# Performance work log

Hardware: AMD Instinct MI355X
Metric: run time of the kernel (lower is better)

The kernel has to match this reference:

```python
import jax, jax.numpy as jnp
import numpy as np

FEAT = 9
H = 128
L = 2
NH = 4
EPS = 1e-5


def _ln(v, g, b):
    m = v.mean(-1, keepdims=True)
    var = ((v - m) ** 2).mean(-1, keepdims=True)
    return (v - m) * jax.lax.rsqrt(var + EPS) * g + b


def _grn(x, fc1_w, fc1_b, fc2_w, fc2_b, gate_w, gate_b, ln_g, ln_b, skip_w=None, skip_b=None):
    h1 = jax.nn.elu(x @ fc1_w.T + fc1_b)
    h = h1 @ fc2_w.T + fc2_b
    g = jax.nn.sigmoid(h1 @ gate_w.T + gate_b)
    s = x if skip_w is None else x @ skip_w.T + skip_b
    return _ln(s + h * g, ln_g, ln_b)


def _lstm(xs, wih, whh, bih, bhh, h0, c0):
    # xs: [B,T,I]; PyTorch gate order i,f,g,o
    pre = jnp.einsum('bti,gi->btg', xs, wih) + bih  # hoist input projection out of scan

    def step(carry, p):
        h, c = carry
        gates = p + h @ whh.T + bhh
        i, f, g, o = jnp.split(gates, 4, axis=-1)
        c = jax.nn.sigmoid(f) * c + jax.nn.sigmoid(i) * jnp.tanh(g)
        h = jax.nn.sigmoid(o) * jnp.tanh(c)
        return (h, c), h

    (h, c), ys = jax.lax.scan(step, (h0, c0), jnp.swapaxes(pre, 0, 1))
    return jnp.swapaxes(ys, 0, 1), h, c


def _mha(q, k, v, in_w, in_b, out_w, out_b):
    B, Tq, _ = q.shape
    Tk = k.shape[1]
    dh = H // NH
    wq, wk, wv = jnp.split(in_w, 3, axis=0)
    bq, bk, bv = jnp.split(in_b, 3, axis=0)
    Q = (q @ wq.T + bq).reshape(B, Tq, NH, dh)
    K = (k @ wk.T + bk).reshape(B, Tk, NH, dh)
    V = (v @ wv.T + bv).reshape(B, Tk, NH, dh)
    a = jnp.einsum('bqhd,bkhd->bhqk', Q, K) * (dh ** -0.5)
    a = jax.nn.softmax(a, axis=-1)
    o = jnp.einsum('bhqk,bkhd->bqhd', a, V).reshape(B, Tq, H)
    return o @ out_w.T + out_b


def _forward(x, vsn_fc1_w, vsn_fc1_b, vsn_fc2_w, vsn_fc2_b, vsn_gate_w, vsn_gate_b,
             vsn_skip_w, vsn_skip_b, vsn_ln_g, vsn_ln_b,
             gc_fc1_w, gc_fc1_b, gc_fc2_w, gc_fc2_b, gc_gate_w, gc_gate_b,
             gc_skip_w, gc_skip_b, gc_ln_g, gc_ln_b,
             enc_wih, enc_whh, enc_bih, enc_bhh,
             dec_wih, dec_whh, dec_bih, dec_bhh,
             attn_in_w, attn_in_b, attn_out_w, attn_out_b,
             pa_fc1_w, pa_fc1_b, pa_fc2_w, pa_fc2_b, pa_gate_w, pa_gate_b, pa_ln_g, pa_ln_b,
             fo_w, fo_b, encoder_steps, forecast_steps):
    B = x.shape[0]
    # --- VariableSelectionNetwork, batched over (batch * time) instead of per-timestep loop ---
    xe = x[:, :encoder_steps, :].reshape(B * encoder_steps, FEAT)  # [N,9]
    # per-feature GRNs with input_dim=1: fc1 weight is a column vector -> broadcast multiply
    h1 = jax.nn.elu(xe[:, :, None] * vsn_fc1_w[None] + vsn_fc1_b[None])  # [N,9,128]
    h = jnp.einsum('nfi,foi->nfo', h1, vsn_fc2_w) + vsn_fc2_b
    g = jax.nn.sigmoid(jnp.einsum('nfi,foi->nfo', h1, vsn_gate_w) + vsn_gate_b)
    s = xe[:, :, None] * vsn_skip_w[None] + vsn_skip_b[None]
    proc = _ln(s + h * g, vsn_ln_g, vsn_ln_b)  # [N,9,128]
    sel = _grn(proc.reshape(-1, FEAT * H), gc_fc1_w, gc_fc1_b, gc_fc2_w, gc_fc2_b,
               gc_gate_w, gc_gate_b, gc_ln_g, gc_ln_b, gc_skip_w, gc_skip_b)  # [N,128]
    enc_in = sel.reshape(B, encoder_steps, H)
    # --- 2-layer encoder LSTM ---
    z = jnp.zeros((B, H), x.dtype)
    y = enc_in
    hs, cs = [], []
    for l in range(L):
        y, hh, cc = _lstm(y, enc_wih[l], enc_whh[l], enc_bih[l], enc_bhh[l], z, z)
        hs.append(hh)
        cs.append(cc)
    enc_out = y  # [B,168,128]
    # --- decoder: last encoder output repeated, init state from encoder ---
    dec_in = jnp.repeat(enc_out[:, -1:, :], forecast_steps, axis=1)
    y = dec_in
    for l in range(L):
        y, _, _ = _lstm(y, dec_wih[l], dec_whh[l], dec_bih[l], dec_bhh[l], hs[l], cs[l])
    # --- cross attention decoder -> encoder ---
    attn = _mha(y, enc_out, enc_out, attn_in_w, attn_in_b, attn_out_w, attn_out_b)
    a = _grn(attn.reshape(-1, H), pa_fc1_w, pa_fc1_b, pa_fc2_w, pa_fc2_b,
             pa_gate_w, pa_gate_b, pa_ln_g, pa_ln_b)
    a = a.reshape(B, forecast_steps, H)
    return a @ fo_w.T + fo_b  # [B,24,6] (6 per-output linears fused)


def setup_inputs() -> dict:
    key = jax.random.key(0)
    ks = iter(jax.random.split(key, 64))

    def rn(*s):
        return jax.random.normal(next(ks), s, dtype=jnp.float32) * 0.05

    B = 256
    return dict(
        x=jax.random.normal(next(ks), (B, 168, FEAT), dtype=jnp.float32),
        vsn_fc1_w=rn(FEAT, H), vsn_fc1_b=rn(FEAT, H),
        vsn_fc2_w=rn(FEAT, H, H), vsn_fc2_b=rn(FEAT, H),
        vsn_gate_w=rn(FEAT, H, H), vsn_gate_b=rn(FEAT, H),
        vsn_skip_w=rn(FEAT, H), vsn_skip_b=rn(FEAT, H),
        vsn_ln_g=jnp.ones((FEAT, H), jnp.float32), vsn_ln_b=jnp.zeros((FEAT, H), jnp.float32),
        gc_fc1_w=rn(H, FEAT * H), gc_fc1_b=rn(H),
        gc_fc2_w=rn(H, H), gc_fc2_b=rn(H),
        gc_gate_w=rn(H, H), gc_gate_b=rn(H),
        gc_skip_w=rn(H, FEAT * H), gc_skip_b=rn(H),
        gc_ln_g=jnp.ones((H,), jnp.float32), gc_ln_b=jnp.zeros((H,), jnp.float32),
        enc_wih=rn(L, 4 * H, H), enc_whh=rn(L, 4 * H, H), enc_bih=rn(L, 4 * H), enc_bhh=rn(L, 4 * H),
        dec_wih=rn(L, 4 * H, H), dec_whh=rn(L, 4 * H, H), dec_bih=rn(L, 4 * H), dec_bhh=rn(L, 4 * H),
        attn_in_w=rn(3 * H, H), attn_in_b=rn(3 * H),
        attn_out_w=rn(H, H), attn_out_b=rn(H),
        pa_fc1_w=rn(H, H), pa_fc1_b=rn(H),
        pa_fc2_w=rn(H, H), pa_fc2_b=rn(H),
        pa_gate_w=rn(H, H), pa_gate_b=rn(H),
        pa_ln_g=jnp.ones((H,), jnp.float32), pa_ln_b=jnp.zeros((H,), jnp.float32),
        fo_w=rn(6, H), fo_b=rn(6),
        encoder_steps=168, forecast_steps=24,
    )


def reference(x, vsn_fc1_w, vsn_fc1_b, vsn_fc2_w, vsn_fc2_b, vsn_gate_w, vsn_gate_b,
              vsn_skip_w, vsn_skip_b, vsn_ln_g, vsn_ln_b,
              gc_fc1_w, gc_fc1_b, gc_fc2_w, gc_fc2_b, gc_gate_w, gc_gate_b,
              gc_skip_w, gc_skip_b, gc_ln_g, gc_ln_b,
              enc_wih, enc_whh, enc_bih, enc_bhh,
              dec_wih, dec_whh, dec_bih, dec_bhh,
              attn_in_w, attn_in_b, attn_out_w, attn_out_b,
              pa_fc1_w, pa_fc1_b, pa_fc2_w, pa_fc2_b, pa_gate_w, pa_gate_b, pa_ln_g, pa_ln_b,
              fo_w, fo_b, encoder_steps, forecast_steps):
    return _forward(x, vsn_fc1_w, vsn_fc1_b, vsn_fc2_w, vsn_fc2_b, vsn_gate_w, vsn_gate_b,
                    vsn_skip_w, vsn_skip_b, vsn_ln_g, vsn_ln_b,
                    gc_fc1_w, gc_fc1_b, gc_fc2_w, gc_fc2_b, gc_gate_w, gc_gate_b,
                    gc_skip_w, gc_skip_b, gc_ln_g, gc_ln_b,
                    enc_wih, enc_whh, enc_bih, enc_bhh,
                    dec_wih, dec_whh, dec_bih, dec_bhh,
                    attn_in_w, attn_in_b, attn_out_w, attn_out_b,
                    pa_fc1_w, pa_fc1_b, pa_fc2_w, pa_fc2_b, pa_gate_w, pa_gate_b, pa_ln_g, pa_ln_b,
                    fo_w, fo_b, encoder_steps, forecast_steps)
```

## Files before the change

### kernel.cpp

```cpp
#include <hip/hip_runtime.h>
#include <hip/hip_bf16.h>

#define NBATCH 256
#define TSE 168
#define TSD 24
#define NTOK (NBATCH*TSE)
#define NDTOK (NBATCH*TSD)

#define OFF_PA_FC1T    0
#define OFF_PA_FC2T    16384
#define OFF_PA_GATET   32768

#define PK_VSN   0
#define PK_GC1   294912
#define PK_GC2   589824
#define PK_ENC0  622592
#define PK_ENC1  688128
#define PK_DEC0  753664
#define PK_DEC1  819200
#define PK_AIN   884736
#define PK_AOUT  933888

typedef __attribute__((ext_vector_type(8))) short short8;
typedef __attribute__((ext_vector_type(4))) float f32x4;
typedef __attribute__((ext_vector_type(2))) __fp16 fp16x2;

__device__ __forceinline__ float sigm(float x){ return 1.f/(1.f + __expf(-x)); }
__device__ __forceinline__ float tanhx(float x){
  float cx = fminf(fmaxf(x, -15.f), 15.f);
  float e = __expf(2.f*cx);
  return (e-1.f)/(e+1.f);
}
__device__ __forceinline__ float eluf(float x){ return x > 0.f ? x : (__expf(x)-1.f); }
__device__ __forceinline__ unsigned short f2bu(float v){
  unsigned int u = __float_as_uint(v);
  u = (u + 0x7fffu + ((u>>16)&1u)) >> 16;
  return (unsigned short)u;
}
__device__ __forceinline__ unsigned int pkh(float a, float b){
  union { fp16x2 h; unsigned int u; } v;
  v.h = __builtin_amdgcn_cvt_pkrtz(a, b);
  return v.u;
}
__device__ __forceinline__ unsigned short f2h(float x){
  union { _Float16 h; unsigned short u; } v;
  v.h = (_Float16)x; return v.u;
}
__device__ __forceinline__ float h2f(unsigned short u){
  union { unsigned short u; _Float16 h; } v;
  v.u = u; return (float)v.h;
}
__device__ __forceinline__ float fd2(unsigned int a, unsigned int b, float c){
  union { unsigned int u; fp16x2 h; } ua, ub;
  ua.u = a; ub.u = b;
  return __builtin_amdgcn_fdot2(ua.h, ub.h, c, false);
}

__global__ __launch_bounds__(256) void k_transpose3(float* __restrict__ wtp,
    const float* s0, const float* s1, const float* s2)
{
  int idx = blockIdx.x*256 + threadIdx.x;
  if (idx >= 49152) return;
  int s = idx >> 14, li = idx & 16383;
  int r = li >> 7, c = li & 127;
  const float* src = (s == 0) ? s0 : (s == 1) ? s1 : s2;
  wtp[s*16384 + c*128 + r] = src[li];
}

__global__ __launch_bounds__(256) void k_pack(
    const float* __restrict__ s0, const float* __restrict__ s1,
    unsigned short* __restrict__ dst, int K, int NC, int nsplit,
    int s0bs, int s1bs, int dstbs)
{
  int id = blockIdx.x*256 + threadIdx.x;
  if (id >= K*NC) return;
  int by = blockIdx.y;
  int n = id / K, k = id - n*K;
  float v = (n < nsplit) ? s0[(size_t)by*s0bs + (size_t)n*K + k]
                         : s1[(size_t)by*s1bs + (size_t)(n-nsplit)*K + k];
  int ct = n >> 4, kc = k >> 5;
  int lane = (n & 15) | (((k >> 3) & 3) << 4);
  int j = k & 7;
  int KC = K >> 5;
  dst[(size_t)by*dstbs + (((size_t)ct*KC + kc)*64 + lane)*8 + j] = f2bu(v);
}

__global__ __launch_bounds__(256) void k_vsn_mfma(
    const float* __restrict__ x, const float* __restrict__ fc1_w, const float* __restrict__ fc1_b,
    const unsigned short* __restrict__ pk, const float* __restrict__ fc2_b,
    const float* __restrict__ gate_b, const float* __restrict__ skip_w,
    const float* __restrict__ skip_b, const float* __restrict__ ln_g,
    const float* __restrict__ ln_b, unsigned short* __restrict__ proc2)
{
  const int f = blockIdx.y;
  const int nb = blockIdx.x;
  const int n0 = nb * 64;
  const int tid = threadIdx.x;
  const int wv = tid >> 6, l = tid & 63;
  __shared__ __align__(16) unsigned short As[64*136];
  __shared__ float xs[64];
  __shared__ float vbuf[64*129];
  __shared__ float red[64][4][2];
  __shared__ float mr[64][2];
  if (tid < 64) xs[tid] = x[(size_t)(n0+tid)*9 + f];
  __syncthreads();
  { int i = tid & 127;
    float w1 = fc1_w[f*128 + i], b1 = fc1_b[f*128 + i];
    for (int it = 0; it < 32; it++) {
      int tk = (tid >> 7) + it*2;
      As[tk*136 + i] = f2bu(eluf(xs[tk]*w1 + b1));
    }
  }
  __syncthreads();
  const unsigned short* Wp = pk + PK_VSN + (size_t)f*32768;
  f32x4 acc[4][4];
  #pragma unroll
  for (int rt = 0; rt < 4; rt++)
    #pragma unroll
    for (int ci = 0; ci < 4; ci++) acc[rt][ci] = (f32x4)(0.f);
  #pragma unroll
  for (int kc = 0; kc < 4; kc++) {
    short8 af[4];
    #pragma unroll
    for (int rt = 0; rt < 4; rt++) {
      int row = rt*16 + (l & 15), g = kc*4 + (l >> 4);
      af[rt] = *(const short8*)&As[row*136 + g*8];
    }
    short8 bf[4];
    #pragma unroll
    for (int ci = 0; ci < 4; ci++) {
      int ct = (ci < 2) ? (wv*2 + ci) : (8 + wv*2 + (ci-2));
      bf[ci] = *(const short8*)&Wp[(((size_t)ct*4 + kc)*64 + l)*8];
    }
    #pragma unroll
    for (int rt = 0; rt < 4; rt++)
      #pragma unroll
      for (int ci = 0; ci < 4; ci++)
        acc[rt][ci] = __builtin_amdgcn_mfma_f32_16x16x32_bf16(af[rt], bf[ci], acc[rt][ci], 0, 0, 0);
  }
  __syncthreads();
  #pragma unroll
  for (int ci = 0; ci < 2; ci++) {
    int ch = wv*32 + ci*16 + (l & 15);
    float fb = fc2_b[f*128 + ch], gb = gate_b[f*128 + ch];
    float sw = skip_w[f*128 + ch], sb = skip_b[f*128 + ch];
    #pragma unroll
    for (int rt = 0; rt < 4; rt++)
      #pragma unroll
      for (int r = 0; r < 4; r++) {
        int row = rt*16 + (l >> 4)*4 + r;
        float hv = acc[rt][ci][r] + fb;
        float gv = sigm(acc[rt][ci+2][r] + gb);
        float sv = xs[row]*sw + sb;
        vbuf[row*129 + ch] = sv + hv*gv;
      }
  }
  __syncthreads();
  { int tk = tid >> 2, q = tid & 3;
    float s1 = 0.f, s2 = 0.f;
    #pragma unroll
    for (int i = 0; i < 32; i++) { float z = vbuf[tk*129 + q*32 + i]; s1 += z; s2 += z*z; }
    red[tk][q][0] = s1; red[tk][q][1] = s2;
  }
  __syncthreads();
  if ((tid & 3) == 0) {
    int tk = tid >> 2;
    float a = 0.f, b2 = 0.f;
    for (int p = 0; p < 4; p++) { a += red[tk][p][0]; b2 += red[tk][p][1]; }
    float mean = a * 0.0078125f;
    float var = b2 * 0.0078125f - mean*mean;
    mr[tk][0] = mean; mr[tk][1] = rsqrtf(fmaxf(var, 0.f) + 1e-5f);
  }
  __syncthreads();
  { int i = tid & 127;
    float lg = ln_g[f*128 + i], lb = ln_b[f*128 + i];
    size_t base = ((size_t)nb*9 + f)*8192;
    for (int it = 0; it < 32; it++) {
      int tk = (tid >> 7) + it*2;
      float z = (vbuf[tk*129 + i] - mr[tk][0]) * mr[tk][1] * lg + lb;
      proc2[base + tk*128 + i] = f2bu(z);
    }
  }
}

__global__ __launch_bounds__(256) void k_gc_mfma(
    const unsigned short* __restrict__ proc2, const unsigned short* __restrict__ pk,
    const float* __restrict__ fc1_b, const float* __restrict__ fc2_b,
    const float* __restrict__ gate_b, const float* __restrict__ skip_b,
    const float* __restrict__ ln_g, const float* __restrict__ ln_b,
    unsigned short* __restrict__ selb)
{
  const int nb = blockIdx.x;
  const int n0 = nb * 64;
  const int tid = threadIdx.x;
  const int wv = tid >> 6, l = tid & 63;
  __shared__ __align__(16) unsigned short As[64*136];
  __shared__ __align__(16) unsigned short A2s[64*136];
  __shared__ float vbuf[64*129];
  __shared__ float red[64][4][2];
  __shared__ float mr[64][2];
  const unsigned short* W1 = pk + PK_GC1;
  f32x4 acc1[4][4];
  #pragma unroll
  for (int rt = 0; rt < 4; rt++)
    #pragma unroll
    for (int ci = 0; ci < 4; ci++) acc1[rt][ci] = (f32x4)(0.f);
  for (int c = 0; c < 9; c++) {
    size_t cbase = ((size_t)nb*9 + c)*8192;
    #pragma unroll
    for (int i = 0; i < 4; i++) {
      int gi = i*256 + tid;
      int row = gi >> 4, g = gi & 15;
      uint4 v = *(const uint4*)(proc2 + cbase + row*128 + g*8);
      *(uint4*)&As[row*136 + g*8] = v;
    }
    __syncthreads();
    #pragma unroll
    for (int kc = 0; kc < 4; kc++) {
      int kk = c*4 + kc;
      short8 af[4];
      #pragma unroll
      for (int rt = 0; rt < 4; rt++) {
        int row = rt*16 + (l & 15), g = kc*4 + (l >> 4);
        af[rt] = *(const short8*)&As[row*136 + g*8];
      }
      short8 bf[4];
      #pragma unroll
      for (int ci = 0; ci < 4; ci++) {
        int ct = (ci < 2) ? (wv*2 + ci) : (8 + wv*2 + (ci-2));
        bf[ci] = *(const short8*)&W1[(((size_t)ct*36 + kk)*64 + l)*8];
      }
      #pragma unroll
      for (int rt = 0; rt < 4; rt++)
        #pragma unroll
        for (int ci = 0; ci < 4; ci++)
          acc1[rt][ci] = __builtin_amdgcn_mfma_f32_16x16x32_bf16(af[rt], bf[ci], acc1[rt][ci], 0, 0, 0);
    }
    __syncthreads();
  }
  #pragma unroll
  for (int ci = 0; ci < 2; ci++) {
    int ch = wv*32 + ci*16 + (l & 15);
    float fb = fc1_b[ch];
    #pragma unroll
    for (int rt = 0; rt < 4; rt++)
      #pragma unroll
      for (int r = 0; r < 4; r++) {
        int row = rt*16 + (l >> 4)*4 + r;
        A2s[row*136 + ch] = f2bu(eluf(acc1[rt][ci][r] + fb));
      }
  }
  __syncthreads();
  const unsigned short* W2 = pk + PK_GC2;
  f32x4 acc2[4][4];
  #pragma unroll
  for (int rt = 0; rt < 4; rt++)
    #pragma unroll
    for (int ci = 0; ci < 4; ci++) acc2[rt][ci] = (f32x4)(0.f);
  #pragma unroll
  for (int kc = 0; kc < 4; kc++) {
    short8 af[4];
    #pragma unroll
    for (int rt = 0; rt < 4; rt++) {
      int row = rt*16 + (l & 15), g = kc*4 + (l >> 4);
      af[rt] = *(const short8*)&A2s[row*136 + g*8];
    }
    short8 bf[4];
    #pragma unroll
    for (int ci = 0; ci < 4; ci++) {
      int ct = (ci < 2) ? (wv*2 + ci) : (8 + wv*2 + (ci-2));
      bf[ci] = *(const short8*)&W2[(((size_t)ct*4 + kc)*64 + l)*8];
    }
    #pragma unroll
    for (int rt = 0; rt < 4; rt++)
      #pragma unroll
      for (int ci = 0; ci < 4; ci++)
        acc2[rt][ci] = __builtin_amdgcn_mfma_f32_16x16x32_bf16(af[rt], bf[ci], acc2[rt][ci], 0, 0, 0);
  }
  __syncthreads();
  #pragma unroll
  for (int ci = 0; ci < 2; ci++) {
    int ch = wv*32 + ci*16 + (l & 15);
    float f2 = fc2_b[ch], gb = gate_b[ch], sb = skip_b[ch];
    #pragma unroll
    for (int rt = 0; rt < 4; rt++)
      #pragma unroll
      for (int r = 0; r < 4; r++) {
        int row = rt*16 + (l >> 4)*4 + r;
        float hv = acc2[rt][ci][r] + f2;
        float gv = sigm(acc2[rt][ci+2][r] + gb);
        float sv = acc1[rt][ci+2][r] + sb;
        vbuf[row*129 + ch] = sv + hv*gv;
      }
  }
  __syncthreads();
  { int tk = tid >> 2, q = tid & 3;
    float s1 = 0.f, s2 = 0.f;
    #pragma unroll
    for (int i = 0; i < 32; i++) { float z = vbuf[tk*129 + q*32 + i]; s1 += z; s2 += z*z; }
    red[tk][q][0] = s1; red[tk][q][1] = s2;
  }
  __syncthreads();
  if ((tid & 3) == 0) {
    int tk = tid >> 2;
    float a = 0.f, b2 = 0.f;
    for (int p = 0; p < 4; p++) { a += red[tk][p][0]; b2 += red[tk][p][1]; }
    float mean = a * 0.0078125f;
    float var = b2 * 0.0078125f - mean*mean;
    mr[tk][0] = mean; mr[tk][1] = rsqrtf(fmaxf(var, 0.f) + 1e-5f);
  }
  __syncthreads();
  { int i = tid & 127;
    float lg = ln_g[i], lb = ln_b[i];
    for (int it = 0; it < 32; it++) {
      int tk = (tid >> 7) + it*2;
      float z = (vbuf[tk*129 + i] - mr[tk][0]) * mr[tk][1] * lg + lb;
      selb[(size_t)(n0+tk)*128 + i] = f2bu(z);
    }
  }
}

__global__ __launch_bounds__(256) void k_mm(
    const unsigned short* __restrict__ A, const unsigned short* __restrict__ Wp,
    const float* __restrict__ b0, const float* __restrict__ b1,
    void* __restrict__ out, int out_ld, int outmode)
{
  const int r0 = blockIdx.x * 64;
  const int cb = blockIdx.y * 128;
  const int tid = threadIdx.x;
  const int wv = tid >> 6, l = tid & 63;
  __shared__ __align__(16) unsigned short As[64*136];
  #pragma unroll
  for (int i = 0; i < 4; i++) {
    int gi = i*256 + tid;
    int row = gi >> 4, g = gi & 15;
    uint4 v = *(const uint4*)(A + (size_t)(r0+row)*128 + g*8);
    *(uint4*)&As[row*136 + g*8] = v;
  }
  __syncthreads();
  f32x4 acc[4][2];
  #pragma unroll
  for (int rt = 0; rt < 4; rt++)
    #pragma unroll
    for (int ci = 0; ci < 2; ci++) acc[rt][ci] = (f32x4)(0.f);
  #pragma unroll
  for (int kc = 0; kc < 4; kc++) {
    short8 af[4];
    #pragma unroll
    for (int rt = 0; rt < 4; rt++) {
      int row = rt*16 + (l & 15), g = kc*4 + (l >> 4);
      af[rt] = *(const short8*)&As[row*136 + g*8];
    }
    short8 bf[2];
    #pragma unroll
    for (int ci = 0; ci < 2; ci++) {
      int ct = (cb >> 4) + wv*2 + ci;
      bf[ci] = *(const short8*)&Wp[(((size_t)ct*4 + kc)*64 + l)*8];
    }
    #pragma unroll
    for (int rt = 0; rt < 4; rt++)
      #pragma unroll
      for (int ci = 0; ci < 2; ci++)
        acc[rt][ci] = __builtin_amdgcn_mfma_f32_16x16x32_bf16(af[rt], bf[ci], acc[rt][ci], 0, 0, 0);
  }
  #pragma unroll
  for (int ci = 0; ci < 2; ci++) {
    int cl = cb + wv*32 + ci*16 + (l & 15);
    float bias = b0[cl] + (b1 ? b1[cl] : 0.f);
    #pragma unroll
    for (int rt = 0; rt < 4; rt++)
      #pragma unroll
      for (int r = 0; r < 4; r++) {
        int row = r0 + rt*16 + (l >> 4)*4 + r;
        float v = acc[rt][ci][r] + bias;
        if (outmode == 0) ((float*)out)[(size_t)row*out_ld + cl] = v;
        else ((unsigned short*)out)[(size_t)row*out_ld + cl] = f2h(v);
      }
  }
}

__global__ __launch_bounds__(256, 1) void k_lscan(
    const unsigned short* __restrict__ pre,
    const float* __restrict__ whh,
    const float* __restrict__ h0i, const float* __restrict__ c0i,
    int T, int tstr,
    unsigned short* __restrict__ ys,
    float* __restrict__ hT, float* __restrict__ cT,
    unsigned short* __restrict__ hTb)
{
  const int b = blockIdx.x, tid = threadIdx.x;
  unsigned int w0[64], w1[64];
  {
    const float* p0 = whh + (size_t)tid*128;
    const float* p1 = whh + (size_t)(tid+256)*128;
    #pragma unroll
    for (int k = 0; k < 64; k++) {
      w0[k] = pkh(p0[2*k], p0[2*k+1]);
      w1[k] = pkh(p1[2*k], p1[2*k+1]);
    }
  }
  __shared__ __align__(16) unsigned short hs[128];
  __shared__ float fg[256];
  float c = 0.f;
  if (tid < 128) {
    float h = h0i ? h0i[(size_t)b*128 + tid] : 0.f;
    c = c0i ? c0i[(size_t)b*128 + tid] : 0.f;
    hs[tid] = f2h(h);
  }
  __syncthreads();
  const unsigned short* preb = pre + (size_t)b * (tstr ? (size_t)T*tstr : 512);
  for (int t = 0; t < T; t++) {
    const unsigned short* pt = preb + (size_t)t*tstr;
    unsigned short p0 = pt[tid], p1 = pt[256 + tid];
    float a0[4] = {0.f,0.f,0.f,0.f}, a1[4] = {0.f,0.f,0.f,0.f};
    #pragma unroll
    for (int k4 = 0; k4 < 16; k4++) {
      uint4 hh = *(const uint4*)&hs[k4*8];
      a0[0] = fd2(w0[4*k4+0], hh.x, a0[0]);
      a0[1] = fd2(w0[4*k4+1], hh.y, a0[1]);
      a0[2] = fd2(w0[4*k4+2], hh.z, a0[2]);
      a0[3] = fd2(w0[4*k4+3], hh.w, a0[3]);
      a1[0] = fd2(w1[4*k4+0], hh.x, a1[0]);
      a1[1] = fd2(w1[4*k4+1], hh.y, a1[1]);
      a1[2] = fd2(w1[4*k4+2], hh.z, a1[2]);
      a1[3] = fd2(w1[4*k4+3], hh.w, a1[3]);
    }
    float g0 = h2f(p0) + (a0[0]+a0[1]) + (a0[2]+a0[3]);
    float g1 = h2f(p1) + (a1[0]+a1[1]) + (a1[2]+a1[3]);
    if (tid >= 128) { fg[tid-128] = g0; fg[tid] = g1; }
    __syncthreads();
    if (tid < 128) {
      float iv = sigm(g0);
      float gv = tanhx(g1);
      float fv = sigm(fg[tid]);
      float ov = sigm(fg[128 + tid]);
      c = fv*c + iv*gv;
      float h = ov * tanhx(c);
      hs[tid] = f2h(h);
      ys[((size_t)b*T + t)*128 + tid] = f2bu(h);
      if (t == T-1) {
        hT[(size_t)b*128 + tid] = h;
        cT[(size_t)b*128 + tid] = c;
        hTb[(size_t)b*128 + tid] = f2bu(h);
      }
    }
    __syncthreads();
  }
}

__global__ __launch_bounds__(256) void k_attn(
    const float* __restrict__ Q, const float* __restrict__ K, const float* __restrict__ V,
    unsigned short* __restrict__ o)
{
  const int b = blockIdx.x, h = blockIdx.y, tid = threadIdx.x;
  __shared__ float Ks[168][33];
  __shared__ float Vs[168][32];
  __shared__ float Qs[24][32];
  __shared__ float Sc[24][169];
  __shared__ float red[24][8];
  __shared__ float rowm[24], rows[24];
  for (int e = tid; e < 168*32; e += 256) {
    int t = e >> 5, d = e & 31;
    Ks[t][d] = K[((size_t)b*168 + t)*128 + h*32 + d];
    Vs[t][d] = V[((size_t)b*168 + t)*128 + h*32 + d];
  }
  for (int e = tid; e < 24*32; e += 256) {
    int q = e >> 5, d = e & 31;
    Qs[q][d] = Q[((size_t)b*24 + q)*128 + h*32 + d];
  }
  __syncthreads();
  for (int e = tid; e < 24*168; e += 256) {
    int q = e / 168, t = e - q*168;
    float s = 0.f;
    #pragma unroll
    for (int d = 0; d < 32; d++) s += Qs[q][d]*Ks[t][d];
    Sc[q][t] = s * 0.17677669529663687f;
  }
  __syncthreads();
  int q = tid >> 3, l8 = tid & 7;
  if (q < 24) {
    float m = -1e30f;
    for (int t = l8; t < 168; t += 8) m = fmaxf(m, Sc[q][t]);
    red[q][l8] = m;
  }
  __syncthreads();
  if (q < 24 && l8 == 0) {
    float m = red[q][0];
    for (int p = 1; p < 8; p++) m = fmaxf(m, red[q][p]);
    rowm[q] = m;
  }
  __syncthreads();
  if (q < 24) {
    float s = 0.f;
    for (int t = l8; t < 168; t += 8) {
      float e2 = __expf(Sc[q][t] - rowm[q]);
      Sc[q][t] = e2; s += e2;
    }
    red[q][l8] = s;
  }
  __syncthreads();
  if (q < 24 && l8 == 0) {
    float s = 0.f;
    for (int p = 0; p < 8; p++) s += red[q][p];
    rows[q] = 1.f/s;
  }
  __syncthreads();
  for (int e = tid; e < 24*32; e += 256) {
    int qq = e >> 5, d = e & 31;
    float acc = 0.f;
    for (int t = 0; t < 168; t++) acc += Sc[qq][t]*Vs[t][d];
    o[((size_t)b*24 + qq)*128 + h*32 + d] = f2bu(acc * rows[qq]);
  }
}

__global__ __launch_bounds__(256) void k_pa_grn(
    const float* __restrict__ xin, const float* __restrict__ wt,
    const float* __restrict__ fc1_b, const float* __restrict__ fc2_b,
    const float* __restrict__ gate_b, const float* __restrict__ ln_g,
    const float* __restrict__ ln_b, float* __restrict__ out)
{
  const int n0 = blockIdx.x * 32;
  const int tid = threadIdx.x;
  __shared__ float xs[32][130];
  __shared__ float h1[32][130];
  __shared__ float red[32][8][2];
  __shared__ float mr[32][2];
  for (int t4 = tid; t4 < 1024; t4 += 256) {
    int r = t4 >> 5, c = (t4 & 31) << 2;
    float4 v = *(const float4*)(xin + (size_t)(n0 + r)*128 + c);
    xs[r][c] = v.x; xs[r][c+1] = v.y; xs[r][c+2] = v.z; xs[r][c+3] = v.w;
  }
  __syncthreads();
  const int oo = tid & 15, tt = tid >> 4;
  const float* fc1t = wt + OFF_PA_FC1T;
  {
    float af[2][8];
    #pragma unroll
    for (int j = 0; j < 2; j++)
      #pragma unroll
      for (int c = 0; c < 8; c++) af[j][c] = 0.f;
    for (int k = 0; k < 128; k++) {
      float4 wa = *(const float4*)(fc1t + k*128 + oo*4);
      float4 wb = *(const float4*)(fc1t + k*128 + 64 + oo*4);
      float wv[8] = {wa.x,wa.y,wa.z,wa.w,wb.x,wb.y,wb.z,wb.w};
      #pragma unroll
      for (int j = 0; j < 2; j++) {
        float a = xs[tt*2+j][k];
        #pragma unroll
        for (int c = 0; c < 8; c++) af[j][c] += a*wv[c];
      }
    }
    #pragma unroll
    for (int j = 0; j < 2; j++) {
      int tk = tt*2 + j;
      #pragma unroll
      for (int c = 0; c < 8; c++) {
        int col = (c < 4) ? (oo*4 + c) : (64 + oo*4 + (c-4));
        h1[tk][col] = eluf(af[j][c] + fc1_b[col]);
      }
    }
  }
  __syncthreads();
  const float* fc2t = wt + OFF_PA_FC2T;
  const float* gtt  = wt + OFF_PA_GATET;
  float ah[2][8], ag[2][8];
  #pragma unroll
  for (int j = 0; j < 2; j++)
    #pragma unroll
    for (int c = 0; c < 8; c++) { ah[j][c] = 0.f; ag[j][c] = 0.f; }
  for (int k = 0; k < 128; k++) {
    float4 wa = *(const float4*)(fc2t + k*128 + oo*4);
    float4 wb = *(const float4*)(fc2t + k*128 + 64 + oo*4);
    float4 wc = *(const float4*)(gtt + k*128 + oo*4);
    float4 wd = *(const float4*)(gtt + k*128 + 64 + oo*4);
    float whv[8] = {wa.x,wa.y,wa.z,wa.w,wb.x,wb.y,wb.z,wb.w};
    float wgv[8] = {wc.x,wc.y,wc.z,wc.w,wd.x,wd.y,wd.z,wd.w};
    #pragma unroll
    for (int j = 0; j < 2; j++) {
      float a = h1[tt*2+j][k];
      #pragma unroll
      for (int c = 0; c < 8; c++) { ah[j][c] += a*whv[c]; ag[j][c] += a*wgv[c]; }
    }
  }
  __syncthreads();
  #pragma unroll
  for (int j = 0; j < 2; j++) {
    int tk = tt*2 + j;
    #pragma unroll
    for (int c = 0; c < 8; c++) {
      int col = (c < 4) ? (oo*4 + c) : (64 + oo*4 + (c-4));
      float hv = ah[j][c] + fc2_b[col];
      float gv = sigm(ag[j][c] + gate_b[col]);
      xs[tk][col] = xs[tk][col] + hv*gv;
    }
  }
  __syncthreads();
  { int tk = tid >> 3, qq = tid & 7;
    float s1 = 0.f, s2 = 0.f;
    #pragma unroll
    for (int i = 0; i < 16; i++) { float z = xs[tk][qq*16+i]; s1 += z; s2 += z*z; }
    red[tk][qq][0] = s1; red[tk][qq][1] = s2;
  }
  __syncthreads();
  if ((tid & 7) == 0) {
    int tk = tid >> 3;
    float a = 0.f, b2 = 0.f;
    for (int p = 0; p < 8; p++) { a += red[tk][p][0]; b2 += red[tk][p][1]; }
    float mean = a * 0.0078125f;
    float var = b2 * 0.0078125f - mean*mean;
    mr[tk][0] = mean; mr[tk][1] = rsqrtf(fmaxf(var, 0.f) + 1e-5f);
  }
  __syncthreads();
  for (int e = tid; e < 32*128; e += 256) {
    int r = e >> 7, c = e & 127;
    out[(size_t)(n0+r)*128 + c] = (xs[r][c] - mr[r][0]) * mr[r][1] * ln_g[c] + ln_b[c];
  }
}

__global__ __launch_bounds__(256) void k_final(
    const float* __restrict__ a, const float* __restrict__ fo_w,
    const float* __restrict__ fo_b, float* __restrict__ out)
{
  int idx = blockIdx.x*256 + threadIdx.x;
  if (idx >= NDTOK*6) return;
  int n = idx / 6, j = idx - n*6;
  const float* ar = a + (size_t)n*128;
  const float* w = fo_w + j*128;
  float s = fo_b[j];
  #pragma unroll 4
  for (int d = 0; d < 128; d++) s += ar[d]*w[d];
  out[idx] = s;
}

extern "C" void kernel_launch(void* const* d_in, const int* in_sizes, int n_in,
                              void* d_out, int out_size, void* d_ws, size_t ws_size,
                              hipStream_t stream) {
  (void)in_sizes; (void)n_in; (void)out_size; (void)ws_size;
  const float* x      = (const float*)d_in[0];
  const float* vfc1w  = (const float*)d_in[1];
  const float* vfc1b  = (const float*)d_in[2];
  const float* vfc2w  = (const float*)d_in[3];
  const float* vfc2b  = (const float*)d_in[4];
  const float* vgw    = (const float*)d_in[5];
  const float* vgb    = (const float*)d_in[6];
  const float* vskw   = (const float*)d_in[7];
  const float* vskb   = (const float*)d_in[8];
  const float* vlng   = (const float*)d_in[9];
  const float* vlnb   = (const float*)d_in[10];
  const float* gfc1w  = (const float*)d_in[11];
  const float* gfc1b  = (const float*)d_in[12];
  const float* gfc2w  = (const float*)d_in[13];
  const float* gfc2b  = (const float*)d_in[14];
  const float* ggw    = (const float*)d_in[15];
  const float* ggb    = (const float*)d_in[16];
  const float* gskw   = (const float*)d_in[17];
  const float* gskb   = (const float*)d_in[18];
  const float* glng   = (const float*)d_in[19];
  const float* glnb   = (const float*)d_in[20];
  const float* encwih = (const float*)d_in[21];
  const float* encwhh = (const float*)d_in[22];
  const float* encbih = (const float*)d_in[23];
  const float* encbhh = (const float*)d_in[24];
  const float* decwih = (const float*)d_in[25];
  const float* decwhh = (const float*)d_in[26];
  const float* decbih = (const float*)d_in[27];
  const float* decbhh = (const float*)d_in[28];
  const float* ainw   = (const float*)d_in[29];
  const float* ainb   = (const float*)d_in[30];
  const float* aoutw  = (const float*)d_in[31];
  const float* aoutb  = (const float*)d_in[32];
  const float* pfc1w  = (const float*)d_in[33];
  const float* pfc1b  = (const float*)d_in[34];
  const float* pfc2w  = (const float*)d_in[35];
  const float* pfc2b  = (const float*)d_in[36];
  const float* pgw    = (const float*)d_in[37];
  const float* pgb    = (const float*)d_in[38];
  const float* plng   = (const float*)d_in[39];
  const float* plnb   = (const float*)d_in[40];
  const float* fow    = (const float*)d_in[41];
  const float* fob    = (const float*)d_in[42];

  float* ws = (float*)d_ws;
  float* wtp = ws;
  unsigned short* pk = (unsigned short*)(ws + 50000);
  unsigned short* proc2 = (unsigned short*)(ws + 530000);
  unsigned short* pre = (unsigned short*)(ws + 530000);
  float* Kb   = ws + 530000;
  float* Vb   = ws + 6100000;
  unsigned short* pre2 = (unsigned short*)(ws + 11700000);
  float* Qb   = ws + 13300000;
  unsigned short* attb = (unsigned short*)(ws + 14100000);
  float* ato  = ws + 14300000;
  float* pao  = ws + 15100000;
  unsigned short* pd0 = (unsigned short*)(ws + 15900000);
  unsigned short* selb  = (unsigned short*)(ws + 25350000);
  unsigned short* encob = (unsigned short*)(ws + 28150000);
  unsigned short* ys0b  = (unsigned short*)(ws + 30950000);
  unsigned short* dys0b = (unsigned short*)(ws + 33750000);
  unsigned short* dout2b = (unsigned short*)(ws + 33950000);
  float* hT0  = ws + 34150000;  float* cT0 = ws + 34190000;
  float* hT1  = ws + 34230000;  float* cT1 = ws + 34270000;
  unsigned short* hT1b = (unsigned short*)(ws + 34310000);
  float* dscr = ws + 34350000;

  k_transpose3<<<dim3(192), dim3(256), 0, stream>>>(wtp, pfc1w, pfc2w, pgw);
  k_pack<<<dim3(128, 9), dim3(256), 0, stream>>>(vfc2w, vgw, pk + PK_VSN, 128, 256, 128, 16384, 16384, 32768);
  k_pack<<<dim3(1152), dim3(256), 0, stream>>>(gfc1w, gskw, pk + PK_GC1, 1152, 256, 128, 0, 0, 0);
  k_pack<<<dim3(128), dim3(256), 0, stream>>>(gfc2w, ggw, pk + PK_GC2, 128, 256, 128, 0, 0, 0);
  k_pack<<<dim3(256), dim3(256), 0, stream>>>(encwih, encwih, pk + PK_ENC0, 128, 512, 512, 0, 0, 0);
  k_pack<<<dim3(256), dim3(256), 0, stream>>>(encwih + 65536, encwih, pk + PK_ENC1, 128, 512, 512, 0, 0, 0);
  k_pack<<<dim3(256), dim3(256), 0, stream>>>(decwih, decwih, pk + PK_DEC0, 128, 512, 512, 0, 0, 0);
  k_pack<<<dim3(256), dim3(256), 0, stream>>>(decwih + 65536, decwih, pk + PK_DEC1, 128, 512, 512, 0, 0, 0);
  k_pack<<<dim3(192), dim3(256), 0, stream>>>(ainw, ainw, pk + PK_AIN, 128, 384, 384, 0, 0, 0);
  k_pack<<<dim3(64), dim3(256), 0, stream>>>(aoutw, aoutw, pk + PK_AOUT, 128, 128, 128, 0, 0, 0);
  k_vsn_mfma<<<dim3(672, 9), dim3(256), 0, stream>>>(x, vfc1w, vfc1b, pk,
      vfc2b, vgb, vskw, vskb, vlng, vlnb, proc2);
  k_gc_mfma<<<dim3(672), dim3(256), 0, stream>>>(proc2, pk, gfc1b, gfc2b, ggb,
      gskb, glng, glnb, selb);
  k_mm<<<dim3(672, 4), dim3(256), 0, stream>>>(selb, pk + PK_ENC0, encbih, encbhh, pre, 512, 1);
  k_lscan<<<dim3(256), dim3(256), 0, stream>>>(pre, encwhh, nullptr, nullptr,
      TSE, 512, ys0b, hT0, cT0, (unsigned short*)dscr);
  k_mm<<<dim3(672, 4), dim3(256), 0, stream>>>(ys0b, pk + PK_ENC1, encbih + 512, encbhh + 512, pre, 512, 1);
  k_lscan<<<dim3(256), dim3(256), 0, stream>>>(pre, encwhh + 65536, nullptr, nullptr,
      TSE, 512, encob, hT1, cT1, hT1b);
  k_mm<<<dim3(4, 4), dim3(256), 0, stream>>>(hT1b, pk + PK_DEC0, decbih, decbhh, pd0, 512, 1);
  k_lscan<<<dim3(256), dim3(256), 0, stream>>>(pd0, decwhh, hT0, cT0,
      TSD, 0, dys0b, dscr + 40000, dscr + 80000, (unsigned short*)dscr);
  k_mm<<<dim3(96, 4), dim3(256), 0, stream>>>(dys0b, pk + PK_DEC1, decbih + 512, decbhh + 512, pre2, 512, 1);
  k_lscan<<<dim3(256), dim3(256), 0, stream>>>(pre2, decwhh + 65536, hT1, cT1,
      TSD, 512, dout2b, dscr + 120000, dscr + 160000, (unsigned short*)dscr);
  k_mm<<<dim3(96, 1), dim3(256), 0, stream>>>(dout2b, pk + PK_AIN, ainb, nullptr, Qb, 128, 0);
  k_mm<<<dim3(672, 1), dim3(256), 0, stream>>>(encob, pk + PK_AIN + 16384, ainb + 128, nullptr, Kb, 128, 0);
  k_mm<<<dim3(672, 1), dim3(256), 0, stream>>>(encob, pk + PK_AIN + 32768, ainb + 256, nullptr, Vb, 128, 0);
  k_attn<<<dim3(256, 4), dim3(256), 0, stream>>>(Qb, Kb, Vb, attb);
  k_mm<<<dim3(96, 1), dim3(256), 0, stream>>>(attb, pk + PK_AOUT, aoutb, nullptr, ato, 128, 0);
  k_pa_grn<<<dim3(192), dim3(256), 0, stream>>>(ato, wtp, pfc1b, pfc2b, pgb,
      plng, plnb, pao);
  k_final<<<dim3(144), dim3(256), 0, stream>>>(pao, fow, fob, (float*)d_out);
}
```

Baseline: 764.5 us.

## Use MFMA for post-attention GRN and one gate per thread in LSTM scan

The post-attention GRN stops using fp32 scalar FMAs over transposed weights. It now uses bf16 MFMA with weights packed by k_pack, and the transpose kernel is removed. Separately, the LSTM recurrent scan now runs 512 threads per block, each computing a single gate row, which halves per-thread register weights and dot-product work per step. The cost is more threads, each holding 64 packed weights, plus bf16 rounding in the GRN.

```diff
diff --git a/kernel.cpp b/kernel.cpp
--- a/kernel.cpp
+++ b/kernel.cpp
@@ -7,19 +7,17 @@
 #define NTOK (NBATCH*TSE)
 #define NDTOK (NBATCH*TSD)
 
-#define OFF_PA_FC1T    0
-#define OFF_PA_FC2T    16384
-#define OFF_PA_GATET   32768
-
-#define PK_VSN   0
-#define PK_GC1   294912
-#define PK_GC2   589824
-#define PK_ENC0  622592
-#define PK_ENC1  688128
-#define PK_DEC0  753664
-#define PK_DEC1  819200
-#define PK_AIN   884736
-#define PK_AOUT  933888
+#define PK_VSN    0
+#define PK_GC1    294912
+#define PK_GC2    589824
+#define PK_ENC0   622592
+#define PK_ENC1   688128
+#define PK_DEC0   753664
+#define PK_DEC1   819200
+#define PK_AIN    884736
+#define PK_AOUT   933888
+#define PK_PAF1   950272
+#define PK_PAF2G  966656
 
 typedef __attribute__((ext_vector_type(8))) short short8;
 typedef __attribute__((ext_vector_type(4))) float f32x4;
@@ -54,17 +52,6 @@
   union { unsigned int u; fp16x2 h; } ua, ub;
   ua.u = a; ub.u = b;
   return __builtin_amdgcn_fdot2(ua.h, ub.h, c, false);
-}
-
-__global__ __launch_bounds__(256) void k_transpose3(float* __restrict__ wtp,
-    const float* s0, const float* s1, const float* s2)
-{
-  int idx = blockIdx.x*256 + threadIdx.x;
-  if (idx >= 49152) return;
-  int s = idx >> 14, li = idx & 16383;
-  int r = li >> 7, c = li & 127;
-  const float* src = (s == 0) ? s0 : (s == 1) ? s1 : s2;
-  wtp[s*16384 + c*128 + r] = src[li];
 }
 
 __global__ __launch_bounds__(256) void k_pack(
@@ -379,7 +366,7 @@
   }
 }
 
-__global__ __launch_bounds__(256, 1) void k_lscan(
+__global__ __launch_bounds__(512, 1) void k_lscan(
     const unsigned short* __restrict__ pre,
     const float* __restrict__ whh,
     const float* __restrict__ h0i, const float* __restrict__ c0i,
@@ -389,18 +376,14 @@
     unsigned short* __restrict__ hTb)
 {
   const int b = blockIdx.x, tid = threadIdx.x;
-  unsigned int w0[64], w1[64];
+  unsigned int w[64];
   {
     const float* p0 = whh + (size_t)tid*128;
-    const float* p1 = whh + (size_t)(tid+256)*128;
-    #pragma unroll
-    for (int k = 0; k < 64; k++) {
-      w0[k] = pkh(p0[2*k], p0[2*k+1]);
-      w1[k] = pkh(p1[2*k], p1[2*k+1]);
-    }
+    #pragma unroll
+    for (int k = 0; k < 64; k++) w[k] = pkh(p0[2*k], p0[2*k+1]);
   }
   __shared__ __align__(16) unsigned short hs[128];
-  __shared__ float fg[256];
+  __shared__ float fg[512];
   float c = 0.f;
   if (tid < 128) {
     float h = h0i ? h0i[(size_t)b*128 + tid] : 0.f;
@@ -410,30 +393,23 @@
   __syncthreads();
   const unsigned short* preb = pre + (size_t)b * (tstr ? (size_t)T*tstr : 512);
   for (int t = 0; t < T; t++) {
-    const unsigned short* pt = preb + (size_t)t*tstr;
-    unsigned short p0 = pt[tid], p1 = pt[256 + tid];
-    float a0[4] = {0.f,0.f,0.f,0.f}, a1[4] = {0.f,0.f,0.f,0.f};
+    unsigned short p = preb[(size_t)t*tstr + tid];
+    float a0 = 0.f, a1 = 0.f, a2 = 0.f, a3 = 0.f;
     #pragma unroll
     for (int k4 = 0; k4 < 16; k4++) {
       uint4 hh = *(const uint4*)&hs[k4*8];
-      a0[0] = fd2(w0[4*k4+0], hh.x, a0[0]);
-      a0[1] = fd2(w0[4*k4+1], hh.y, a0[1]);
-      a0[2] = fd2(w0[4*k4+2], hh.z, a0[2]);
-      a0[3] = fd2(w0[4*k4+3], hh.w, a0[3]);
-      a1[0] = fd2(w1[4*k4+0], hh.x, a1[0]);
-      a1[1] = fd2(w1[4*k4+1], hh.y, a1[1]);
-      a1[2] = fd2(w1[4*k4+2], hh.z, a1[2]);
-      a1[3] = fd2(w1[4*k4+3], hh.w, a1[3]);
-    }
-    float g0 = h2f(p0) + (a0[0]+a0[1]) + (a0[2]+a0[3]);
-    float g1 = h2f(p1) + (a1[0]+a1[1]) + (a1[2]+a1[3]);
-    if (tid >= 128) { fg[tid-128] = g0; fg[tid] = g1; }
+      a0 = fd2(w[4*k4+0], hh.x, a0);
+      a1 = fd2(w[4*k4+1], hh.y, a1);
+      a2 = fd2(w[4*k4+2], hh.z, a2);
+      a3 = fd2(w[4*k4+3], hh.w, a3);
+    }
+    fg[tid] = h2f(p) + (a0+a1) + (a2+a3);
     __syncthreads();
     if (tid < 128) {
-      float iv = sigm(g0);
-      float gv = tanhx(g1);
-      float fv = sigm(fg[tid]);
-      float ov = sigm(fg[128 + tid]);
+      float iv = sigm (fg[tid]);
+      float fv = sigm (fg[128 + tid]);
+      float gv = tanhx(fg[256 + tid]);
+      float ov = sigm (fg[384 + tid]);
       c = fv*c + iv*gv;
       float h = ov * tanhx(c);
       hs[tid] = f2h(h);
@@ -513,107 +489,134 @@
   }
 }
 
-__global__ __launch_bounds__(256) void k_pa_grn(
-    const float* __restrict__ xin, const float* __restrict__ wt,
+__global__ __launch_bounds__(256) void k_pa_mfma(
+    const float* __restrict__ xin, const unsigned short* __restrict__ pk,
     const float* __restrict__ fc1_b, const float* __restrict__ fc2_b,
     const float* __restrict__ gate_b, const float* __restrict__ ln_g,
     const float* __restrict__ ln_b, float* __restrict__ out)
 {
-  const int n0 = blockIdx.x * 32;
+  const int n0 = blockIdx.x * 64;
   const int tid = threadIdx.x;
-  __shared__ float xs[32][130];
-  __shared__ float h1[32][130];
-  __shared__ float red[32][8][2];
-  __shared__ float mr[32][2];
-  for (int t4 = tid; t4 < 1024; t4 += 256) {
-    int r = t4 >> 5, c = (t4 & 31) << 2;
-    float4 v = *(const float4*)(xin + (size_t)(n0 + r)*128 + c);
-    xs[r][c] = v.x; xs[r][c+1] = v.y; xs[r][c+2] = v.z; xs[r][c+3] = v.w;
-  }
-  __syncthreads();
-  const int oo = tid & 15, tt = tid >> 4;
-  const float* fc1t = wt + OFF_PA_FC1T;
-  {
-    float af[2][8];
-    #pragma unroll
-    for (int j = 0; j < 2; j++)
-      #pragma unroll
-      for (int c = 0; c < 8; c++) af[j][c] = 0.f;
-    for (int k = 0; k < 128; k++) {
-      float4 wa = *(const float4*)(fc1t + k*128 + oo*4);
-      float4 wb = *(const float4*)(fc1t + k*128 + 64 + oo*4);
-      float wv[8] = {wa.x,wa.y,wa.z,wa.w,wb.x,wb.y,wb.z,wb.w};
-      #pragma unroll
-      for (int j = 0; j < 2; j++) {
-        float a = xs[tt*2+j][k];
-        #pragma unroll
-        for (int c = 0; c < 8; c++) af[j][c] += a*wv[c];
-      }
-    }
-    #pragma unroll
-    for (int j = 0; j < 2; j++) {
-      int tk = tt*2 + j;
-      #pragma unroll
-      for (int c = 0; c < 8; c++) {
-        int col = (c < 4) ? (oo*4 + c) : (64 + oo*4 + (c-4));
-        h1[tk][col] = eluf(af[j][c] + fc1_b[col]);
-      }
-    }
-  }
-  __syncthreads();
-  const float* fc2t = wt + OFF_PA_FC2T;
-  const float* gtt  = wt + OFF_PA_GATET;
-  float ah[2][8], ag[2][8];
-  #pragma unroll
-  for (int j = 0; j < 2; j++)
-    #pragma unroll
-    for (int c = 0; c < 8; c++) { ah[j][c] = 0.f; ag[j][c] = 0.f; }
-  for (int k = 0; k < 128; k++) {
-    float4 wa = *(const float4*)(fc2t + k*128 + oo*4);
-    float4 wb = *(const float4*)(fc2t + k*128 + 64 + oo*4);
-    float4 wc = *(const float4*)(gtt + k*128 + oo*4);
-    float4 wd = *(const float4*)(gtt + k*128 + 64 + oo*4);
-    float whv[8] = {wa.x,wa.y,wa.z,wa.w,wb.x,wb.y,wb.z,wb.w};
-    float wgv[8] = {wc.x,wc.y,wc.z,wc.w,wd.x,wd.y,wd.z,wd.w};
-    #pragma unroll
-    for (int j = 0; j < 2; j++) {
-      float a = h1[tt*2+j][k];
-      #pragma unroll
-      for (int c = 0; c < 8; c++) { ah[j][c] += a*whv[c]; ag[j][c] += a*wgv[c]; }
-    }
-  }
-  __syncthreads();
-  #pragma unroll
-  for (int j = 0; j < 2; j++) {
-    int tk = tt*2 + j;
-    #pragma unroll
-    for (int c = 0; c < 8; c++) {
-      int col = (c < 4) ? (oo*4 + c) : (64 + oo*4 + (c-4));
-      float hv = ah[j][c] + fc2_b[col];
-      float gv = sigm(ag[j][c] + gate_b[col]);
-      xs[tk][col] = xs[tk][col] + hv*gv;
-    }
-  }
-  __syncthreads();
-  { int tk = tid >> 3, qq = tid & 7;
+  const int wv = tid >> 6, l = tid & 63;
+  __shared__ __align__(16) unsigned short As[64*136];
+  __shared__ __align__(16) unsigned short A2s[64*136];
+  __shared__ float xs[64*129];
+  __shared__ float red[64][4][2];
+  __shared__ float mr[64][2];
+  for (int i2 = 0; i2 < 8; i2++) {
+    int t4 = i2*256 + tid;
+    int r = t4 >> 5, cc = (t4 & 31) << 2;
+    float4 v = *(const float4*)(xin + (size_t)(n0 + r)*128 + cc);
+    xs[r*129 + cc] = v.x; xs[r*129 + cc+1] = v.y;
+    xs[r*129 + cc+2] = v.z; xs[r*129 + cc+3] = v.w;
+    As[r*136 + cc] = f2bu(v.x); As[r*136 + cc+1] = f2bu(v.y);
+    As[r*136 + cc+2] = f2bu(v.z); As[r*136 + cc+3] = f2bu(v.w);
+  }
+  __syncthreads();
+  const unsigned short* W1 = pk + PK_PAF1;
+  f32x4 acc1[4][2];
+  #pragma unroll
+  for (int rt = 0; rt < 4; rt++)
+    #pragma unroll
+    for (int ci = 0; ci < 2; ci++) acc1[rt][ci] = (f32x4)(0.f);
+  #pragma unroll
+  for (int kc = 0; kc < 4; kc++) {
+    short8 af[4];
+    #pragma unroll
+    for (int rt = 0; rt < 4; rt++) {
+      int row = rt*16 + (l & 15), g = kc*4 + (l >> 4);
+      af[rt] = *(const short8*)&As[row*136 + g*8];
+    }
+    short8 bf[2];
+    #pragma unroll
+    for (int ci = 0; ci < 2; ci++) {
+      int ct = wv*2 + ci;
+      bf[ci] = *(const short8*)&W1[(((size_t)ct*4 + kc)*64 + l)*8];
+    }
+    #pragma unroll
+    for (int rt = 0; rt < 4; rt++)
+      #pragma unroll
+      for (int ci = 0; ci < 2; ci++)
+        acc1[rt][ci] = __builtin_amdgcn_mfma_f32_16x16x32_bf16(af[rt], bf[ci], acc1[rt][ci], 0, 0, 0);
+  }
+  __syncthreads();
+  #pragma unroll
+  for (int ci = 0; ci < 2; ci++) {
+    int ch = wv*32 + ci*16 + (l & 15);
+    float fb = fc1_b[ch];
+    #pragma unroll
+    for (int rt = 0; rt < 4; rt++)
+      #pragma unroll
+      for (int r = 0; r < 4; r++) {
+        int row = rt*16 + (l >> 4)*4 + r;
+        A2s[row*136 + ch] = f2bu(eluf(acc1[rt][ci][r] + fb));
+      }
+  }
+  __syncthreads();
+  const unsigned short* W2 = pk + PK_PAF2G;
+  f32x4 acc2[4][4];
+  #pragma unroll
+  for (int rt = 0; rt < 4; rt++)
+    #pragma unroll
+    for (int ci = 0; ci < 4; ci++) acc2[rt][ci] = (f32x4)(0.f);
+  #pragma unroll
+  for (int kc = 0; kc < 4; kc++) {
+    short8 af[4];
+    #pragma unroll
+    for (int rt = 0; rt < 4; rt++) {
+      int row = rt*16 + (l & 15), g = kc*4 + (l >> 4);
+      af[rt] = *(const short8*)&A2s[row*136 + g*8];
+    }
+    short8 bf[4];
+    #pragma unroll
+    for (int ci = 0; ci < 4; ci++) {
+      int ct = (ci < 2) ? (wv*2 + ci) : (8 + wv*2 + (ci-2));
+      bf[ci] = *(const short8*)&W2[(((size_t)ct*4 + kc)*64 + l)*8];
+    }
+    #pragma unroll
+    for (int rt = 0; rt < 4; rt++)
+      #pragma unroll
+      for (int ci = 0; ci < 4; ci++)
+        acc2[rt][ci] = __builtin_amdgcn_mfma_f32_16x16x32_bf16(af[rt], bf[ci], acc2[rt][ci], 0, 0, 0);
+  }
+  __syncthreads();
+  #pragma unroll
+  for (int ci = 0; ci < 2; ci++) {
+    int ch = wv*32 + ci*16 + (l & 15);
+    float f2 = fc2_b[ch], gb = gate_b[ch];
+    #pragma unroll
+    for (int rt = 0; rt < 4; rt++)
+      #pragma unroll
+      for (int r = 0; r < 4; r++) {
+        int row = rt*16 + (l >> 4)*4 + r;
+        float hv = acc2[rt][ci][r] + f2;
+        float gv = sigm(acc2[rt][ci+2][r] + gb);
+        xs[row*129 + ch] = xs[row*129 + ch] + hv*gv;
+      }
+  }
+  __syncthreads();
+  { int tk = tid >> 2, q = tid & 3;
     float s1 = 0.f, s2 = 0.f;
     #pragma unroll
-    for (int i = 0; i < 16; i++) { float z = xs[tk][qq*16+i]; s1 += z; s2 += z*z; }
-    red[tk][qq][0] = s1; red[tk][qq][1] = s2;
-  }
-  __syncthreads();
-  if ((tid & 7) == 0) {
-    int tk = tid >> 3;
+    for (int i = 0; i < 32; i++) { float z = xs[tk*129 + q*32 + i]; s1 += z; s2 += z*z; }
+    red[tk][q][0] = s1; red[tk][q][1] = s2;
+  }
+  __syncthreads();
+  if ((tid & 3) == 0) {
+    int tk = tid >> 2;
     float a = 0.f, b2 = 0.f;
-    for (int p = 0; p < 8; p++) { a += red[tk][p][0]; b2 += red[tk][p][1]; }
+    for (int p = 0; p < 4; p++) { a += red[tk][p][0]; b2 += red[tk][p][1]; }
     float mean = a * 0.0078125f;
     float var = b2 * 0.0078125f - mean*mean;
     mr[tk][0] = mean; mr[tk][1] = rsqrtf(fmaxf(var, 0.f) + 1e-5f);
   }
   __syncthreads();
-  for (int e = tid; e < 32*128; e += 256) {
-    int r = e >> 7, c = e & 127;
-    out[(size_t)(n0+r)*128 + c] = (xs[r][c] - mr[r][0]) * mr[r][1] * ln_g[c] + ln_b[c];
+  { int i = tid & 127;
+    float lg = ln_g[i], lb = ln_b[i];
+    for (int it = 0; it < 32; it++) {
+      int tk = (tid >> 7) + it*2;
+      out[(size_t)(n0+tk)*128 + i] = (xs[tk*129 + i] - mr[tk][0]) * mr[tk][1] * lg + lb;
+    }
   }
 }
 
@@ -681,8 +684,7 @@
   const float* fob    = (const float*)d_in[42];
 
   float* ws = (float*)d_ws;
-  float* wtp = ws;
-  unsigned short* pk = (unsigned short*)(ws + 50000);
+  unsigned short* pk = (unsigned short*)ws;
   unsigned short* proc2 = (unsigned short*)(ws + 530000);
   unsigned short* pre = (unsigned short*)(ws + 530000);
   float* Kb   = ws + 530000;
@@ -703,7 +705,6 @@
   unsigned short* hT1b = (unsigned short*)(ws + 34310000);
   float* dscr = ws + 34350000;
 
-  k_transpose3<<<dim3(192), dim3(256), 0, stream>>>(wtp, pfc1w, pfc2w, pgw);
   k_pack<<<dim3(128, 9), dim3(256), 0, stream>>>(vfc2w, vgw, pk + PK_VSN, 128, 256, 128, 16384, 16384, 32768);
   k_pack<<<dim3(1152), dim3(256), 0, stream>>>(gfc1w, gskw, pk + PK_GC1, 1152, 256, 128, 0, 0, 0);
   k_pack<<<dim3(128), dim3(256), 0, stream>>>(gfc2w, ggw, pk + PK_GC2, 128, 256, 128, 0, 0, 0);
@@ -713,28 +714,30 @@
   k_pack<<<dim3(256), dim3(256), 0, stream>>>(decwih + 65536, decwih, pk + PK_DEC1, 128, 512, 512, 0, 0, 0);
   k_pack<<<dim3(192), dim3(256), 0, stream>>>(ainw, ainw, pk + PK_AIN, 128, 384, 384, 0, 0, 0);
   k_pack<<<dim3(64), dim3(256), 0, stream>>>(aoutw, aoutw, pk + PK_AOUT, 128, 128, 128, 0, 0, 0);
+  k_pack<<<dim3(64), dim3(256), 0, stream>>>(pfc1w, pfc1w, pk + PK_PAF1, 128, 128, 128, 0, 0, 0);
+  k_pack<<<dim3(128), dim3(256), 0, stream>>>(pfc2w, pgw, pk + PK_PAF2G, 128, 256, 128, 0, 0, 0);
   k_vsn_mfma<<<dim3(672, 9), dim3(256), 0, stream>>>(x, vfc1w, vfc1b, pk,
       vfc2b, vgb, vskw, vskb, vlng, vlnb, proc2);
   k_gc_mfma<<<dim3(672), dim3(256), 0, stream>>>(proc2, pk, gfc1b, gfc2b, ggb,
       gskb, glng, glnb, selb);
   k_mm<<<dim3(672, 4), dim3(256), 0, stream>>>(selb, pk + PK_ENC0, encbih, encbhh, pre, 512, 1);
-  k_lscan<<<dim3(256), dim3(256), 0, stream>>>(pre, encwhh, nullptr, nullptr,
+  k_lscan<<<dim3(256), dim3(512), 0, stream>>>(pre, encwhh, nullptr, nullptr,
       TSE, 512, ys0b, hT0, cT0, (unsigned short*)dscr);
   k_mm<<<dim3(672, 4), dim3(256), 0, stream>>>(ys0b, pk + PK_ENC1, encbih + 512, encbhh + 512, pre, 512, 1);
-  k_lscan<<<dim3(256), dim3(256), 0, stream>>>(pre, encwhh + 65536, nullptr, nullptr,
+  k_lscan<<<dim3(256), dim3(512), 0, stream>>>(pre, encwhh + 65536, nullptr, nullptr,
       TSE, 512, encob, hT1, cT1, hT1b);
   k_mm<<<dim3(4, 4), dim3(256), 0, stream>>>(hT1b, pk + PK_DEC0, decbih, decbhh, pd0, 512, 1);
-  k_lscan<<<dim3(256), dim3(256), 0, stream>>>(pd0, decwhh, hT0, cT0,
+  k_lscan<<<dim3(256), dim3(512), 0, stream>>>(pd0, decwhh, hT0, cT0,
       TSD, 0, dys0b, dscr + 40000, dscr + 80000, (unsigned short*)dscr);
   k_mm<<<dim3(96, 4), dim3(256), 0, stream>>>(dys0b, pk + PK_DEC1, decbih + 512, decbhh + 512, pre2, 512, 1);
-  k_lscan<<<dim3(256), dim3(256), 0, stream>>>(pre2, decwhh + 65536, hT1, cT1,
+  k_lscan<<<dim3(256), dim3(512), 0, stream>>>(pre2, decwhh + 65536, hT1, cT1,
       TSD, 512, dout2b, dscr + 120000, dscr + 160000, (unsigned short*)dscr);
   k_mm<<<dim3(96, 1), dim3(256), 0, stream>>>(dout2b, pk + PK_AIN, ainb, nullptr, Qb, 128, 0);
   k_mm<<<dim3(672, 1), dim3(256), 0, stream>>>(encob, pk + PK_AIN + 16384, ainb + 128, nullptr, Kb, 128, 0);
   k_mm<<<dim3(672, 1), dim3(256), 0, stream>>>(encob, pk + PK_AIN + 32768, ainb + 256, nullptr, Vb, 128, 0);
   k_attn<<<dim3(256, 4), dim3(256), 0, stream>>>(Qb, Kb, Vb, attb);
   k_mm<<<dim3(96, 1), dim3(256), 0, stream>>>(attb, pk + PK_AOUT, aoutb, nullptr, ato, 128, 0);
-  k_pa_grn<<<dim3(192), dim3(256), 0, stream>>>(ato, wtp, pfc1b, pfc2b, pgb,
+  k_pa_mfma<<<dim3(96), dim3(256), 0, stream>>>(ato, pk, pfc1b, pfc2b, pgb,
       plng, plnb, pao);
   k_final<<<dim3(144), dim3(256), 0, stream>>>(pao, fow, fob, (float*)d_out);
 }
```

Measured after the change: 739.1 us, median of 2. 1.03x faster.
